# Kernel optimization log

Measured on AMD Instinct MI355X. Metric: run time of the kernel, lower is better.

The kernel has to match this reference:

```python
import jax, jax.numpy as jnp
import numpy as np

N = 400000
CIN = 16
COUT = 32
K = 9  # taps in a (1,3,3) or (3,1,3) kernel
EPS = 1e-5


def subm_conv(feat, nbr, W):
    """Submanifold sparse conv as gather-matmul-scatter.
    feat: [N, C]; nbr: [N, K] indices in [0, N] (N == missing -> zero); W: [K, C, O].
    """
    feat_pad = jnp.concatenate([feat, jnp.zeros((1, feat.shape[1]), feat.dtype)], axis=0)
    g = feat_pad[nbr]                       # [N, K, C] irregular gather
    return jnp.einsum('nkc,kco->no', g, W)  # [N, O]


def bn_relu(x, gamma, beta, mean, var):
    # eval-mode BatchNorm1d over channel dim + ReLU
    return jax.nn.relu((x - mean) * jax.lax.rsqrt(var + EPS) * gamma + beta)


def setup_inputs() -> dict:
    key = jax.random.key(0)
    ks = jax.random.split(key, 8)
    features = jax.random.normal(ks[0], (N, CIN), jnp.float32)
    nbr13 = jax.random.randint(ks[1], (N, K), 0, N + 1, jnp.int32)
    nbr31 = jax.random.randint(ks[2], (N, K), 0, N + 1, jnp.int32)
    w1 = jax.random.normal(ks[3], (K, CIN, COUT), jnp.float32) * 0.05
    w12 = jax.random.normal(ks[4], (K, COUT, COUT), jnp.float32) * 0.05
    w2 = jax.random.normal(ks[5], (K, CIN, COUT), jnp.float32) * 0.05
    w3 = jax.random.normal(ks[6], (K, COUT, COUT), jnp.float32) * 0.05
    gamma = jax.random.uniform(ks[7], (4, COUT), jnp.float32, 0.5, 1.5)
    beta = jnp.zeros((4, COUT), jnp.float32)
    mean = jnp.zeros((4, COUT), jnp.float32)
    var = jnp.ones((4, COUT), jnp.float32)
    return dict(features=features, nbr13=nbr13, nbr31=nbr31,
                w1=w1, w12=w12, w2=w2, w3=w3,
                gamma=gamma, beta=beta, mean=mean, var=var)


def reference(features, nbr13, nbr31, w1, w12, w2, w3, gamma, beta, mean, var):
    # shortcut branch: conv1x3 -> BN -> ReLU -> conv3x1 -> BN -> ReLU
    sc = bn_relu(subm_conv(features, nbr13, w1), gamma[0], beta[0], mean[0], var[0])
    sc = bn_relu(subm_conv(sc, nbr31, w12), gamma[1], beta[1], mean[1], var[1])
    # main branch: conv3x1 -> BN -> ReLU -> conv1x3 -> BN -> ReLU
    out = bn_relu(subm_conv(features, nbr31, w2), gamma[2], beta[2], mean[2], var[2])
    out = bn_relu(subm_conv(out, nbr13, w3), gamma[3], beta[3], mean[3], var[3])
    return out + sc
```

## Files before the change

### kernel.cpp

```cpp
#include <hip/hip_runtime.h>

#define NPTS 400000
#define KTAPS 9
#define BN_EPS 1e-5f
#define NTILES (NPTS / 16)

typedef __attribute__((ext_vector_type(8))) short bf16x8;
typedef __attribute__((ext_vector_type(4))) float f32x4;

__device__ __forceinline__ unsigned short f2bf(float f) {
    union { float f; unsigned int i; } v; v.f = f;
    v.i += 0x7fffu + ((v.i >> 16) & 1u);
    return (unsigned short)(v.i >> 16);
}

__global__ __launch_bounds__(256) void cvt_feat(const float* __restrict__ feat,
                                                unsigned short* __restrict__ fb) {
    int n = blockIdx.x * 256 + threadIdx.x;
    if (n >= NPTS) return;
    const float4* p = reinterpret_cast<const float4*>(feat + (size_t)n * 16);
    float4 a = p[0], b = p[1], c = p[2], d = p[3];
    float v[16] = {a.x,a.y,a.z,a.w, b.x,b.y,b.z,b.w,
                   c.x,c.y,c.z,c.w, d.x,d.y,d.z,d.w};
    unsigned int pk[8];
    #pragma unroll
    for (int j = 0; j < 8; ++j)
        pk[j] = (unsigned int)f2bf(v[2*j]) | ((unsigned int)f2bf(v[2*j+1]) << 16);
    uint4* o = reinterpret_cast<uint4*>(fb + (size_t)n * 16);
    o[0] = make_uint4(pk[0], pk[1], pk[2], pk[3]);
    o[1] = make_uint4(pk[4], pk[5], pk[6], pk[7]);
}

template<int CIN, bool ADD, bool OUT_BF16>
__global__ __launch_bounds__(256) void conv_mfma(
    const unsigned short* __restrict__ tab,
    const int* __restrict__ nbr,
    const float* __restrict__ W,
    const float* __restrict__ gam, const float* __restrict__ bet,
    const float* __restrict__ mea, const float* __restrict__ var,
    void* __restrict__ outp)
{
    constexpr int NFRAG = (CIN == 16) ? 5 : 9;
    __shared__ __align__(16) unsigned short Bp[NFRAG * 2 * 512];

    const int tid = threadIdx.x;
    for (int f = tid; f < NFRAG * 1024; f += 256) {
        int j = f & 7, l = (f >> 3) & 63, fb = f >> 9;
        int g = fb >> 1, b = fb & 1;
        int kk = 8 * (l >> 4) + j;
        int tap, ch;
        if (CIN == 16) { tap = 2 * g + (kk >> 4); ch = kk & 15; }
        else           { tap = g;                 ch = kk;      }
        float w = (tap < KTAPS) ? W[((size_t)tap * CIN + ch) * 32 + b * 16 + (l & 15)] : 0.f;
        Bp[f] = f2bf(w);
    }
    __syncthreads();

    const int lane = tid & 63;
    const int lrow = lane & 15, lgrp = lane >> 4;
    const int nwaves = gridDim.x * 4;

    for (int tile = blockIdx.x * 4 + (tid >> 6); tile < NTILES; tile += nwaves) {
        const int tb = tile * 16;
        const int prow = tb + lrow;

        int idx[KTAPS];
        #pragma unroll
        for (int k = 0; k < KTAPS; ++k) idx[k] = nbr[(size_t)prow * KTAPS + k];

        uint4 ga[NFRAG];
        #pragma unroll
        for (int q = 0; q < NFRAG; ++q) {
            int tsel, boff;
            if (CIN == 16) { tsel = 2 * q + (lgrp >> 1); if (tsel > 8) tsel = 8;
                             boff = (lgrp & 1) * 16; }
            else           { tsel = q; boff = lgrp * 16; }
            int id = idx[tsel];
            int s = (id < NPTS) ? id : 0;
            uint4 gv = *reinterpret_cast<const uint4*>(
                reinterpret_cast<const char*>(tab) + (size_t)s * (CIN * 2) + boff);
            if (id >= NPTS) gv = make_uint4(0u, 0u, 0u, 0u);
            ga[q] = gv;
        }

        f32x4 acc0 = {0.f, 0.f, 0.f, 0.f}, acc1 = {0.f, 0.f, 0.f, 0.f};
        #pragma unroll
        for (int q = 0; q < NFRAG; ++q) {
            bf16x8 a  = *reinterpret_cast<const bf16x8*>(&ga[q]);
            bf16x8 b0 = *reinterpret_cast<const bf16x8*>(&Bp[(2*q + 0) * 512 + lane * 8]);
            bf16x8 b1 = *reinterpret_cast<const bf16x8*>(&Bp[(2*q + 1) * 512 + lane * 8]);
            acc0 = __builtin_amdgcn_mfma_f32_16x16x32_bf16(a, b0, acc0, 0, 0, 0);
            acc1 = __builtin_amdgcn_mfma_f32_16x16x32_bf16(a, b1, acc1, 0, 0, 0);
        }

        #pragma unroll
        for (int b = 0; b < 2; ++b) {
            const int o = b * 16 + lrow;
            const float s  = gam[o] * rsqrtf(var[o] + BN_EPS);
            const float bb = bet[o] - mea[o] * s;
            const f32x4 a = (b == 0) ? acc0 : acc1;
            #pragma unroll
            for (int r = 0; r < 4; ++r) {
                const int m = tb + 4 * lgrp + r;
                float y = fmaxf(fmaf(a[r], s, bb), 0.f);
                if (OUT_BF16) {
                    ((unsigned short*)outp)[(size_t)m * 32 + o] = f2bf(y);
                } else {
                    float* po = (float*)outp + (size_t)m * 32 + o;
                    if (ADD) y += *po;
                    *po = y;
                }
            }
        }
    }
}

extern "C" void kernel_launch(void* const* d_in, const int* in_sizes, int n_in,
                              void* d_out, int out_size, void* d_ws, size_t ws_size,
                              hipStream_t stream) {
    const float* features = (const float*)d_in[0];
    const int*   nbr13    = (const int*)  d_in[1];
    const int*   nbr31    = (const int*)  d_in[2];
    const float* w1       = (const float*)d_in[3];
    const float* w12      = (const float*)d_in[4];
    const float* w2       = (const float*)d_in[5];
    const float* w3       = (const float*)d_in[6];
    const float* gamma    = (const float*)d_in[7];
    const float* beta     = (const float*)d_in[8];
    const float* mean     = (const float*)d_in[9];
    const float* var      = (const float*)d_in[10];
    float* out = (float*)d_out;

    unsigned short* sc1 = (unsigned short*)d_ws;
    unsigned short* tmn = (unsigned short*)d_ws + (size_t)NPTS * 32;
    unsigned short* fb  = (unsigned short*)d_out;

    cvt_feat<<<(NPTS + 255) / 256, 256, 0, stream>>>(features, fb);

    conv_mfma<16, false, true><<<2048, 256, 0, stream>>>(
        fb, nbr13, w1, gamma + 0,  beta + 0,  mean + 0,  var + 0,  sc1);
    conv_mfma<16, false, true><<<2048, 256, 0, stream>>>(
        fb, nbr31, w2, gamma + 64, beta + 64, mean + 64, var + 64, tmn);
    conv_mfma<32, false, false><<<2048, 256, 0, stream>>>(
        tmn, nbr13, w3, gamma + 96, beta + 96, mean + 96, var + 96, out);
    conv_mfma<32, true, false><<<2048, 256, 0, stream>>>(
        sc1, nbr31, w12, gamma + 32, beta + 32, mean + 32, var + 32, out);
}
```

Before: 298.8 us.

## Prepack bf16 weights and BN scales once, launch one tile per wave

A new pack_all kernel converts all four weight tensors to the MFMA bf16 fragment layout and folds the BN scale/bias once. Each conv block then copies these with uint4 loads, or falls back to in-kernel packing if the workspace is too small. The grid-stride loop is replaced by one 16-row tile per wave (NTILES/4 blocks), so neighbor index loads are issued before the LDS fill and barrier and overlap with it. In exchange there are many more blocks, each repeating the weight copy into LDS, plus one extra small launch.

```diff
diff --git a/kernel.cpp b/kernel.cpp
--- a/kernel.cpp
+++ b/kernel.cpp
@@ -31,85 +31,127 @@
     o[1] = make_uint4(pk[4], pk[5], pk[6], pk[7]);
 }
 
-template<int CIN, bool ADD, bool OUT_BF16>
-__global__ __launch_bounds__(256) void conv_mfma(
-    const unsigned short* __restrict__ tab,
-    const int* __restrict__ nbr,
-    const float* __restrict__ W,
-    const float* __restrict__ gam, const float* __restrict__ bet,
-    const float* __restrict__ mea, const float* __restrict__ var,
-    void* __restrict__ outp)
+__global__ __launch_bounds__(256) void pack_all(
+    const float* __restrict__ w1, const float* __restrict__ w2,
+    const float* __restrict__ w12, const float* __restrict__ w3,
+    const float* __restrict__ gamma, const float* __restrict__ beta,
+    const float* __restrict__ mean, const float* __restrict__ var,
+    unsigned short* __restrict__ pw, float* __restrict__ sbf)
 {
-    constexpr int NFRAG = (CIN == 16) ? 5 : 9;
-    __shared__ __align__(16) unsigned short Bp[NFRAG * 2 * 512];
-
-    const int tid = threadIdx.x;
-    for (int f = tid; f < NFRAG * 1024; f += 256) {
+    int t = blockIdx.x * 256 + threadIdx.x;
+    if (t < 28672) {
+        const float* W; int CIN, f;
+        if      (t < 5120)  { W = w1;  CIN = 16; f = t; }
+        else if (t < 10240) { W = w2;  CIN = 16; f = t - 5120; }
+        else if (t < 19456) { W = w12; CIN = 32; f = t - 10240; }
+        else                { W = w3;  CIN = 32; f = t - 19456; }
         int j = f & 7, l = (f >> 3) & 63, fb = f >> 9;
         int g = fb >> 1, b = fb & 1;
         int kk = 8 * (l >> 4) + j;
         int tap, ch;
         if (CIN == 16) { tap = 2 * g + (kk >> 4); ch = kk & 15; }
         else           { tap = g;                 ch = kk;      }
-        float w = (tap < KTAPS) ? W[((size_t)tap * CIN + ch) * 32 + b * 16 + (l & 15)] : 0.f;
-        Bp[f] = f2bf(w);
-    }
-    __syncthreads();
-
+        float w = (tap < KTAPS) ? W[((size_t)(tap * CIN + ch)) * 32 + b * 16 + (l & 15)] : 0.f;
+        pw[t] = f2bf(w);
+    } else if (t < 28672 + 128) {
+        int r = t - 28672;
+        float s  = gamma[r] * rsqrtf(var[r] + BN_EPS);
+        float bb = beta[r] - mean[r] * s;
+        sbf[2 * r]     = s;
+        sbf[2 * r + 1] = bb;
+    }
+}
+
+template<int CIN, bool ADD, bool OUT_BF16>
+__global__ __launch_bounds__(256) void conv_mfma(
+    const unsigned short* __restrict__ tab,
+    const int* __restrict__ nbr,
+    const float* __restrict__ Wf32,
+    const unsigned short* __restrict__ pW,
+    const float* __restrict__ sbf,
+    const float* __restrict__ gam, const float* __restrict__ bet,
+    const float* __restrict__ mea, const float* __restrict__ var,
+    void* __restrict__ outp)
+{
+    constexpr int NFRAG = (CIN == 16) ? 5 : 9;
+    __shared__ __align__(16) unsigned short Bp[NFRAG * 1024];
+    __shared__ float2 SB[32];
+
+    const int tid  = threadIdx.x;
     const int lane = tid & 63;
     const int lrow = lane & 15, lgrp = lane >> 4;
-    const int nwaves = gridDim.x * 4;
-
-    for (int tile = blockIdx.x * 4 + (tid >> 6); tile < NTILES; tile += nwaves) {
-        const int tb = tile * 16;
-        const int prow = tb + lrow;
-
-        int idx[KTAPS];
+    const int tile = blockIdx.x * 4 + (tid >> 6);
+    const int tb   = tile * 16;
+    const int prow = tb + lrow;
+
+    int idx[KTAPS];
+    #pragma unroll
+    for (int k = 0; k < KTAPS; ++k) idx[k] = nbr[(size_t)prow * KTAPS + k];
+
+    if (pW != nullptr) {
         #pragma unroll
-        for (int k = 0; k < KTAPS; ++k) idx[k] = nbr[(size_t)prow * KTAPS + k];
-
-        uint4 ga[NFRAG];
+        for (int i = tid; i < NFRAG * 128; i += 256)
+            reinterpret_cast<uint4*>(Bp)[i] = reinterpret_cast<const uint4*>(pW)[i];
+        if (tid < 32) SB[tid] = reinterpret_cast<const float2*>(sbf)[tid];
+    } else {
+        for (int f = tid; f < NFRAG * 1024; f += 256) {
+            int j = f & 7, l = (f >> 3) & 63, fb = f >> 9;
+            int g = fb >> 1, b = fb & 1;
+            int kk = 8 * (l >> 4) + j;
+            int tap, ch;
+            if (CIN == 16) { tap = 2 * g + (kk >> 4); ch = kk & 15; }
+            else           { tap = g;                 ch = kk;      }
+            float w = (tap < KTAPS) ? Wf32[((size_t)(tap * CIN + ch)) * 32 + b * 16 + (l & 15)] : 0.f;
+            Bp[f] = f2bf(w);
+        }
+        if (tid < 32) {
+            float s  = gam[tid] * rsqrtf(var[tid] + BN_EPS);
+            float bb = bet[tid] - mea[tid] * s;
+            SB[tid] = make_float2(s, bb);
+        }
+    }
+    __syncthreads();
+
+    uint4 ga[NFRAG];
+    #pragma unroll
+    for (int q = 0; q < NFRAG; ++q) {
+        int tsel, boff;
+        if (CIN == 16) { tsel = 2 * q + (lgrp >> 1); if (tsel > 8) tsel = 8;
+                         boff = (lgrp & 1) * 16; }
+        else           { tsel = q; boff = lgrp * 16; }
+        int id = idx[tsel];
+        int s = (id < NPTS) ? id : 0;
+        uint4 gv = *reinterpret_cast<const uint4*>(
+            reinterpret_cast<const char*>(tab) + (size_t)s * (CIN * 2) + boff);
+        if (id >= NPTS) gv = make_uint4(0u, 0u, 0u, 0u);
+        ga[q] = gv;
+    }
+
+    f32x4 acc0 = {0.f, 0.f, 0.f, 0.f}, acc1 = {0.f, 0.f, 0.f, 0.f};
+    #pragma unroll
+    for (int q = 0; q < NFRAG; ++q) {
+        bf16x8 a  = *reinterpret_cast<const bf16x8*>(&ga[q]);
+        bf16x8 b0 = *reinterpret_cast<const bf16x8*>(&Bp[(2*q + 0) * 512 + lane * 8]);
+        bf16x8 b1 = *reinterpret_cast<const bf16x8*>(&Bp[(2*q + 1) * 512 + lane * 8]);
+        acc0 = __builtin_amdgcn_mfma_f32_16x16x32_bf16(a, b0, acc0, 0, 0, 0);
+        acc1 = __builtin_amdgcn_mfma_f32_16x16x32_bf16(a, b1, acc1, 0, 0, 0);
+    }
+
+    #pragma unroll
+    for (int b = 0; b < 2; ++b) {
+        const int o = b * 16 + lrow;
+        const float2 sv = SB[o];
+        const f32x4 a = (b == 0) ? acc0 : acc1;
         #pragma unroll
-        for (int q = 0; q < NFRAG; ++q) {
-            int tsel, boff;
-            if (CIN == 16) { tsel = 2 * q + (lgrp >> 1); if (tsel > 8) tsel = 8;
-                             boff = (lgrp & 1) * 16; }
-            else           { tsel = q; boff = lgrp * 16; }
-            int id = idx[tsel];
-            int s = (id < NPTS) ? id : 0;
-            uint4 gv = *reinterpret_cast<const uint4*>(
-                reinterpret_cast<const char*>(tab) + (size_t)s * (CIN * 2) + boff);
-            if (id >= NPTS) gv = make_uint4(0u, 0u, 0u, 0u);
-            ga[q] = gv;
-        }
-
-        f32x4 acc0 = {0.f, 0.f, 0.f, 0.f}, acc1 = {0.f, 0.f, 0.f, 0.f};
-        #pragma unroll
-        for (int q = 0; q < NFRAG; ++q) {
-            bf16x8 a  = *reinterpret_cast<const bf16x8*>(&ga[q]);
-            bf16x8 b0 = *reinterpret_cast<const bf16x8*>(&Bp[(2*q + 0) * 512 + lane * 8]);
-            bf16x8 b1 = *reinterpret_cast<const bf16x8*>(&Bp[(2*q + 1) * 512 + lane * 8]);
-            acc0 = __builtin_amdgcn_mfma_f32_16x16x32_bf16(a, b0, acc0, 0, 0, 0);
-            acc1 = __builtin_amdgcn_mfma_f32_16x16x32_bf16(a, b1, acc1, 0, 0, 0);
-        }
-
-        #pragma unroll
-        for (int b = 0; b < 2; ++b) {
-            const int o = b * 16 + lrow;
-            const float s  = gam[o] * rsqrtf(var[o] + BN_EPS);
-            const float bb = bet[o] - mea[o] * s;
-            const f32x4 a = (b == 0) ? acc0 : acc1;
-            #pragma unroll
-            for (int r = 0; r < 4; ++r) {
-                const int m = tb + 4 * lgrp + r;
-                float y = fmaxf(fmaf(a[r], s, bb), 0.f);
-                if (OUT_BF16) {
-                    ((unsigned short*)outp)[(size_t)m * 32 + o] = f2bf(y);
-                } else {
-                    float* po = (float*)outp + (size_t)m * 32 + o;
-                    if (ADD) y += *po;
-                    *po = y;
-                }
+        for (int r = 0; r < 4; ++r) {
+            const int m = tb + 4 * lgrp + r;
+            float y = fmaxf(fmaf(a[r], sv.x, sv.y), 0.f);
+            if (OUT_BF16) {
+                ((unsigned short*)outp)[(size_t)m * 32 + o] = f2bf(y);
+            } else {
+                float* po = (float*)outp + (size_t)m * 32 + o;
+                if (ADD) y += *po;
+                *po = y;
             }
         }
     }
@@ -131,18 +173,39 @@
     const float* var      = (const float*)d_in[10];
     float* out = (float*)d_out;
 
+    const size_t tabShorts = (size_t)NPTS * 32;
     unsigned short* sc1 = (unsigned short*)d_ws;
-    unsigned short* tmn = (unsigned short*)d_ws + (size_t)NPTS * 32;
+    unsigned short* tmn = sc1 + tabShorts;
     unsigned short* fb  = (unsigned short*)d_out;
 
+    unsigned short* pw  = nullptr;
+    float*          sbf = nullptr;
+    const size_t need = 2 * tabShorts * 2 + 28672 * 2 + 256 * 4;
+    if (ws_size >= need) {
+        pw  = tmn + tabShorts;
+        sbf = (float*)(pw + 28672);
+        pack_all<<<113, 256, 0, stream>>>(w1, w2, w12, w3, gamma, beta, mean, var, pw, sbf);
+    }
+
     cvt_feat<<<(NPTS + 255) / 256, 256, 0, stream>>>(features, fb);
 
-    conv_mfma<16, false, true><<<2048, 256, 0, stream>>>(
-        fb, nbr13, w1, gamma + 0,  beta + 0,  mean + 0,  var + 0,  sc1);
-    conv_mfma<16, false, true><<<2048, 256, 0, stream>>>(
-        fb, nbr31, w2, gamma + 64, beta + 64, mean + 64, var + 64, tmn);
-    conv_mfma<32, false, false><<<2048, 256, 0, stream>>>(
-        tmn, nbr13, w3, gamma + 96, beta + 96, mean + 96, var + 96, out);
-    conv_mfma<32, true, false><<<2048, 256, 0, stream>>>(
-        sc1, nbr31, w12, gamma + 32, beta + 32, mean + 32, var + 32, out);
-}
+    const unsigned short* pw1  = pw;
+    const unsigned short* pw2  = pw ? pw + 5120  : nullptr;
+    const unsigned short* pw12 = pw ? pw + 10240 : nullptr;
+    const unsigned short* pw3  = pw ? pw + 19456 : nullptr;
+
+    dim3 grid(NTILES / 4), block(256);
+
+    conv_mfma<16, false, true><<<grid, block, 0, stream>>>(
+        fb, nbr13, w1, pw1, sbf ? sbf + 0 : nullptr,
+        gamma + 0,  beta + 0,  mean + 0,  var + 0,  sc1);
+    conv_mfma<16, false, true><<<grid, block, 0, stream>>>(
+        fb, nbr31, w2, pw2, sbf ? sbf + 128 : nullptr,
+        gamma + 64, beta + 64, mean + 64, var + 64, tmn);
+    conv_mfma<32, false, false><<<grid, block, 0, stream>>>(
+        tmn, nbr13, w3, pw3, sbf ? sbf + 192 : nullptr,
+        gamma + 96, beta + 96, mean + 96, var + 96, out);
+    conv_mfma<32, true, false><<<grid, block, 0, stream>>>(
+        sc1, nbr31, w12, pw12, sbf ? sbf + 64 : nullptr,
+        gamma + 32, beta + 32, mean + 32, var + 32, out);
+}
```

Result: faster. 262.6 us (-12.1%).
